# Performance work log

Hardware: AMD Instinct MI355X
Metric: run time of the kernel (lower is better)

## Reference

```python
import jax, jax.numpy as jnp
import numpy as np

N_HEAD = 16
MAX_WAVELENGTH = 10000
ROPE_PCT = 1.0


def apply_p_rope(inputs, positions, head_dim, max_wavelength=MAX_WAVELENGTH, rope_percentage=ROPE_PCT):
    # inputs: [..., T, D], positions: [T]
    rope_angles = int(rope_percentage * head_dim // 2)
    nope_angles = head_dim // 2 - rope_angles
    fraction = 2.0 * jnp.arange(0, rope_angles) / head_dim
    timescale = max_wavelength ** fraction
    timescale = jnp.pad(timescale, (0, nope_angles), mode='constant', constant_values=(0, jnp.inf))
    sinusoid_inp = positions[..., None] / timescale[None, :]  # [T, D/2]
    sin = jnp.sin(sinusoid_inp)
    cos = jnp.cos(sinusoid_inp)
    first_half, second_half = jnp.split(inputs, 2, axis=-1)
    first_part = first_half * cos - second_half * sin
    second_part = second_half * cos + first_half * sin
    return jnp.concatenate([first_part, second_part], axis=-1).astype(inputs.dtype)


def setup_inputs() -> dict:
    key = jax.random.key(0)
    ks = jax.random.split(key, 4)
    B, T, C = 2, 2048, 1024
    x = jax.random.normal(ks[0], (B, T, C), dtype=jnp.float32)
    W_attn = jax.random.normal(ks[1], (C, 3 * C), dtype=jnp.float32) * 0.02
    b_attn = jnp.zeros((3 * C,), dtype=jnp.float32)
    W_proj = jax.random.normal(ks[2], (C, C), dtype=jnp.float32) * 0.02
    b_proj = jnp.zeros((C,), dtype=jnp.float32)
    return {"x": x, "W_attn": W_attn, "b_attn": b_attn, "W_proj": W_proj, "b_proj": b_proj}


def reference(x, W_attn, b_attn, W_proj, b_proj):
    B, T, C = x.shape
    H = N_HEAD
    D = C // H  # head_dim
    qkv = x @ W_attn + b_attn                     # [B, T, 3C]
    q, k, v = jnp.split(qkv, 3, axis=-1)
    def split_heads(t):
        return t.reshape(B, T, H, D).transpose(0, 2, 1, 3)  # [B, H, T, D]
    q, k, v = split_heads(q), split_heads(k), split_heads(v)
    positions = jnp.arange(T, dtype=q.dtype)
    q = apply_p_rope(q, positions, D)
    k = apply_p_rope(k, positions, D)
    scale = jnp.sqrt(D).astype(k.dtype)
    attn = jnp.einsum('bhqd,bhkd->bhqk', q, k) / scale  # [B, H, T, T]
    causal_mask = jnp.tril(jnp.ones((T, T))).astype(bool)
    attn = jnp.where(causal_mask, attn, jnp.finfo(attn.dtype).min)
    attn = jax.nn.softmax(attn, axis=-1)
    y = jnp.einsum('bhqk,bhkd->bhqd', attn, v)    # [B, H, T, D]
    y = y.transpose(0, 2, 1, 3).reshape(B, T, C)
    return y @ W_proj + b_proj
```

## Files before the change

### kernel.cpp

```cpp
#include <hip/hip_runtime.h>
#include <hip/hip_bf16.h>

typedef short short8 __attribute__((ext_vector_type(8)));
typedef float f32x4 __attribute__((ext_vector_type(4)));
typedef __hip_bfloat16 bf16;

#define MFMA(a, b, c) __builtin_amdgcn_mfma_f32_16x16x32_bf16(a, b, c, 0, 0, 0)
#define EXP2(x) __builtin_amdgcn_exp2f(x)

__device__ __forceinline__ void async16(const void* g, void* l) {
  __builtin_amdgcn_global_load_lds((const __attribute__((address_space(1))) void*)g,
                                   (__attribute__((address_space(3))) void*)l, 16, 0, 0);
}

__device__ __forceinline__ short f2bs(float x) {
  bf16 h = __float2bfloat16(x);
  return __builtin_bit_cast(short, h);
}
__device__ __forceinline__ unsigned pk2(float lo, float hi) {
  return ((unsigned)(unsigned short)f2bs(hi) << 16) | (unsigned)(unsigned short)f2bs(lo);
}

__launch_bounds__(256)
__global__ void prep(const float* __restrict__ Wa, bf16* __restrict__ WaT,
                     const float* __restrict__ Wp, bf16* __restrict__ WpT,
                     const float* __restrict__ x, bf16* __restrict__ xb,
                     float2* __restrict__ tab) {
  __shared__ __align__(16) short Ts[64 * 72];
  int id = blockIdx.x;
  int tid = threadIdx.x;
  if (id < 1024) {
    const float* src; bf16* dst; int R, Cc, bx, by;
    if (id < 768) { src = Wa; dst = WaT; R = 1024; Cc = 3072; bx = id % 48; by = id / 48; }
    else { int r = id - 768; src = Wp; dst = WpT; R = 1024; Cc = 1024; bx = r & 15; by = r >> 4; }
    int r0 = by * 64, c0 = bx * 64;
#pragma unroll
    for (int c = 0; c < 4; ++c) {
      int g = c * 1024 + tid * 4;
      int rr = g >> 6, cc = g & 63;
      float4 v = *(const float4*)(src + (size_t)(r0 + rr) * Cc + c0 + cc);
      Ts[rr * 72 + cc + 0] = f2bs(v.x);
      Ts[rr * 72 + cc + 1] = f2bs(v.y);
      Ts[rr * 72 + cc + 2] = f2bs(v.z);
      Ts[rr * 72 + cc + 3] = f2bs(v.w);
    }
    __syncthreads();
#pragma unroll
    for (int c = 0; c < 2; ++c) {
      int g = c * 2048 + tid * 8;
      int co = g >> 6, ro = g & 63;
      short8 vv;
#pragma unroll
      for (int jj = 0; jj < 8; ++jj) vv[jj] = Ts[(ro + jj) * 72 + co];
      *(short8*)(dst + (size_t)(c0 + co) * R + r0 + ro) = vv;
    }
  } else {
    int cid = id - 1024;
    int i0 = (cid * 256 + tid) * 8;
    float4 a = *(const float4*)(x + i0);
    float4 b = *(const float4*)(x + i0 + 4);
    short8 o;
    o[0] = f2bs(a.x); o[1] = f2bs(a.y); o[2] = f2bs(a.z); o[3] = f2bs(a.w);
    o[4] = f2bs(b.x); o[5] = f2bs(b.y); o[6] = f2bs(b.z); o[7] = f2bs(b.w);
    *(short8*)((short*)xb + i0) = o;
    if (cid < 256) {
      int idx = cid * 256 + tid;
      int t = idx >> 5, d = idx & 31;
      float inv = powf(10000.0f, -(float)d * (1.0f / 32.0f));
      float ang = (float)t * inv;
      tab[idx] = make_float2(cosf(ang), sinf(ang));
    }
  }
}

__launch_bounds__(256)
__global__ void gemm_qkv(const bf16* __restrict__ A, const bf16* __restrict__ Bt,
                         const float* __restrict__ bias,
                         const float2* __restrict__ rope,
                         bf16* __restrict__ qp, bf16* __restrict__ kp,
                         bf16* __restrict__ vp) {
  const int K = 1024;
  __shared__ __align__(16) short As[128 * 32];
  __shared__ __align__(16) short Bs[128 * 32];
  int tid = threadIdx.x;
  int lane = tid & 63, wave = tid >> 6;
  int l = lane & 15, quad = lane >> 4;
  int wm = wave & 1, wn = wave >> 1;
  int mBase = blockIdx.y * 128, nBase = blockIdx.x * 128;

  f32x4 acc[4][4] = {};

  int r0 = tid >> 2;
  int kk = (tid & 3) * 8;
  const bf16* Ap = A + (size_t)(mBase + r0) * K + kk;
  const bf16* Bp = Bt + (size_t)(nBase + r0) * K + kk;
  short* Asp = As + tid * 8;
  short* Bsp = Bs + tid * 8;

  for (int kb = 0; kb < K / 32; ++kb) {
    __syncthreads();
    async16(Ap, Asp);
    async16(Ap + (size_t)64 * K, Asp + 2048);
    async16(Bp, Bsp);
    async16(Bp + (size_t)64 * K, Bsp + 2048);
    Ap += 32; Bp += 32;
    __syncthreads();
    short8 af[4], bfr[4];
#pragma unroll
    for (int i = 0; i < 4; ++i)
      af[i] = *(const short8*)(As + (wm * 64 + i * 16 + l) * 32 + quad * 8);
#pragma unroll
    for (int j = 0; j < 4; ++j)
      bfr[j] = *(const short8*)(Bs + (wn * 64 + j * 16 + l) * 32 + quad * 8);
#pragma unroll
    for (int i = 0; i < 4; ++i)
#pragma unroll
      for (int j = 0; j < 4; ++j)
        acc[i][j] = MFMA(af[i], bfr[j], acc[i][j]);
  }

  int nsec = nBase + wn * 64;
  float bv[4];
#pragma unroll
  for (int j = 0; j < 4; ++j) bv[j] = bias[nsec + j * 16 + l];

  int sel = nsec >> 10;
  int h = (nsec & 1023) >> 6;
  if (sel < 2) {
    bf16* dst = (sel == 0) ? qp : kp;
    float mul = (sel == 0) ? 0.18033688f : 1.0f;
#pragma unroll
    for (int i = 0; i < 4; ++i) {
#pragma unroll
      for (int reg = 0; reg < 4; ++reg) {
        int m = mBase + wm * 64 + i * 16 + quad * 4 + reg;
        int t = m & 2047, b = m >> 11;
        size_t base = ((size_t)((b * 16 + h) * 2048 + t)) * 64;
#pragma unroll
        for (int j = 0; j < 2; ++j) {
          int d = j * 16 + l;
          float x1 = acc[i][j][reg] + bv[j];
          float x2 = acc[i][j + 2][reg] + bv[j + 2];
          float2 cs = rope[t * 32 + d];
          dst[base + d]      = __float2bfloat16((x1 * cs.x - x2 * cs.y) * mul);
          dst[base + d + 32] = __float2bfloat16((x2 * cs.x + x1 * cs.y) * mul);
        }
      }
    }
  } else {
#pragma unroll
    for (int i = 0; i < 4; ++i) {
      int m0 = mBase + wm * 64 + i * 16 + quad * 4;
      int t0 = m0 & 2047, b = m0 >> 11;
#pragma unroll
      for (int j = 0; j < 4; ++j) {
        int d = j * 16 + l;
        uint2 uu;
        uu.x = pk2(acc[i][j][0] + bv[j], acc[i][j][1] + bv[j]);
        uu.y = pk2(acc[i][j][2] + bv[j], acc[i][j][3] + bv[j]);
        *(uint2*)(vp + ((size_t)((b * 16 + h) * 64 + d)) * 2048 + t0) = uu;
      }
    }
  }
}

__launch_bounds__(256)
__global__ void gemm_proj(const bf16* __restrict__ A, const bf16* __restrict__ Bt,
                          const float* __restrict__ bias, float* __restrict__ out) {
  const int K = 1024, Nn = 1024;
  __shared__ __align__(16) short As[64 * 32];
  __shared__ __align__(16) short Bs[128 * 32];
  int tid = threadIdx.x;
  int lane = tid & 63, wave = tid >> 6;
  int l = lane & 15, quad = lane >> 4;
  int mBase = blockIdx.y * 64, nBase = blockIdx.x * 128;

  f32x4 acc[4][2] = {};

  int r0 = tid >> 2;
  int kk = (tid & 3) * 8;
  const bf16* Ap = A + (size_t)(mBase + r0) * K + kk;
  const bf16* Bp = Bt + (size_t)(nBase + r0) * K + kk;
  short* Asp = As + tid * 8;
  short* Bsp = Bs + tid * 8;

  for (int kb = 0; kb < K / 32; ++kb) {
    __syncthreads();
    async16(Ap, Asp);
    async16(Bp, Bsp);
    async16(Bp + (size_t)64 * K, Bsp + 2048);
    Ap += 32; Bp += 32;
    __syncthreads();
    short8 af[4], bfr[2];
#pragma unroll
    for (int i = 0; i < 4; ++i)
      af[i] = *(const short8*)(As + (i * 16 + l) * 32 + quad * 8);
#pragma unroll
    for (int j = 0; j < 2; ++j)
      bfr[j] = *(const short8*)(Bs + (wave * 32 + j * 16 + l) * 32 + quad * 8);
#pragma unroll
    for (int i = 0; i < 4; ++i)
#pragma unroll
      for (int j = 0; j < 2; ++j)
        acc[i][j] = MFMA(af[i], bfr[j], acc[i][j]);
  }

  int nsec = nBase + wave * 32;
  float bv[2];
#pragma unroll
  for (int j = 0; j < 2; ++j) bv[j] = bias[nsec + j * 16 + l];
#pragma unroll
  for (int i = 0; i < 4; ++i)
#pragma unroll
    for (int reg = 0; reg < 4; ++reg) {
      int m = mBase + i * 16 + quad * 4 + reg;
#pragma unroll
      for (int j = 0; j < 2; ++j)
        out[(size_t)m * Nn + nsec + j * 16 + l] = acc[i][j][reg] + bv[j];
    }
}

__launch_bounds__(256)
__global__ void flash_attn(const bf16* __restrict__ q, const bf16* __restrict__ k,
                           const bf16* __restrict__ vt, bf16* __restrict__ y) {
  __shared__ __align__(16) short Ps[4 * 32 * 66];
  int tid = threadIdx.x;
  int lane = tid & 63, wave = tid >> 6;
  int l = lane & 15, quad = lane >> 4;
  int bh = blockIdx.x;
  int by = blockIdx.y;
  int qi = (by < 8) ? (15 - by) : (by - 8);
  int q0 = qi * 128;
  int bb = bh >> 4, hh = bh & 15;

  const bf16* qh = q + (size_t)bh * 2048 * 64;
  const bf16* kh = k + (size_t)bh * 2048 * 64;
  const bf16* vh = vt + (size_t)bh * 64 * 2048;

  int qrb = q0 + wave * 32;

  short8 qf[2][2];
#pragma unroll
  for (int m = 0; m < 2; ++m)
#pragma unroll
    for (int ks = 0; ks < 2; ++ks)
      qf[m][ks] = *(const short8*)(qh + (size_t)(qrb + m * 16 + l) * 64 + ks * 32 + quad * 8);

  const bf16* kfp = kh + (size_t)l * 64 + quad * 8;
  const bf16* vfp = vh + (size_t)l * 2048 + quad * 8;

  f32x4 acc[2][4] = {};
  float lr[2][4] = {{0.f, 0.f, 0.f, 0.f}, {0.f, 0.f, 0.f, 0.f}};
  short* Pw = Ps + wave * (32 * 66);
  int nkt = ((qrb + 31) >> 6) + 1;

  for (int kt = 0; kt < nkt; ++kt) {
    int kv0 = kt * 64;

    short8 kf[2][4];
#pragma unroll
    for (int ks = 0; ks < 2; ++ks)
#pragma unroll
      for (int jn = 0; jn < 4; ++jn)
        kf[ks][jn] = *(const short8*)(kfp + (size_t)(kv0 + jn * 16) * 64 + ks * 32);

    f32x4 sacc[2][4];
#pragma unroll
    for (int m = 0; m < 2; ++m)
#pragma unroll
      for (int jn = 0; jn < 4; ++jn) sacc[m][jn] = f32x4{-16.f, -16.f, -16.f, -16.f};
    bool live1 = (kv0 <= qrb + 31);
#pragma unroll
    for (int ks = 0; ks < 2; ++ks)
#pragma unroll
      for (int jn = 0; jn < 4; ++jn) {
        sacc[0][jn] = MFMA(qf[0][ks], kf[ks][jn], sacc[0][jn]);
        sacc[1][jn] = MFMA(qf[1][ks], kf[ks][jn], sacc[1][jn]);
      }

    short8 vf[2][4];
#pragma unroll
    for (int ks = 0; ks < 2; ++ks)
#pragma unroll
      for (int jd = 0; jd < 4; ++jd)
        vf[ks][jd] = *(const short8*)(vfp + (size_t)(jd * 16) * 2048 + kv0 + ks * 32);

#pragma unroll
    for (int m = 0; m < 2; ++m) {
      int qlo = qrb + m * 16;
      if (m == 0 && kv0 > qlo + 15) continue;
      bool nm = (kv0 + 63) > qlo;
#pragma unroll
      for (int reg = 0; reg < 4; ++reg) {
        int qg = qlo + quad * 4 + reg;
        int prow = (m * 16 + quad * 4 + reg) * 66 + l;
        float ps = 0.f;
#pragma unroll
        for (int jn = 0; jn < 4; ++jn) {
          float s = sacc[m][jn][reg];
          if (nm) s = (kv0 + jn * 16 + l <= qg) ? s : -1e30f;
          float p = EXP2(s);
          ps += p;
          Pw[prow + jn * 16] = f2bs(p);
        }
        lr[m][reg] += ps;
      }
    }

#pragma unroll
    for (int m = 0; m < 2; ++m) {
      if (m == 0 && kv0 > qrb + 15) continue;
      if (m == 1 && !live1) continue;
#pragma unroll
      for (int ks = 0; ks < 2; ++ks) {
        short8 pf = *(const short8*)(Pw + (m * 16 + l) * 66 + ks * 32 + quad * 8);
#pragma unroll
        for (int jd = 0; jd < 4; ++jd)
          acc[m][jd] = MFMA(pf, vf[ks][jd], acc[m][jd]);
      }
    }
  }

#pragma unroll
  for (int m = 0; m < 2; ++m) {
#pragma unroll
    for (int reg = 0; reg < 4; ++reg) {
      float s = lr[m][reg];
#pragma unroll
      for (int mm = 1; mm <= 8; mm <<= 1)
        s += __shfl_xor(s, mm, 64);
      float inv = 1.0f / s;
      int t = qrb + m * 16 + quad * 4 + reg;
      size_t yb = ((size_t)(bb * 2048 + t)) * 1024 + hh * 64;
#pragma unroll
      for (int jd = 0; jd < 4; ++jd)
        y[yb + jd * 16 + l] = __float2bfloat16(acc[m][jd][reg] * inv);
    }
  }
}

extern "C" void kernel_launch(void* const* d_in, const int* in_sizes, int n_in,
                              void* d_out, int out_size, void* d_ws, size_t ws_size,
                              hipStream_t stream) {
  const float* x  = (const float*)d_in[0];
  const float* Wa = (const float*)d_in[1];
  const float* ba = (const float*)d_in[2];
  const float* Wp = (const float*)d_in[3];
  const float* bp = (const float*)d_in[4];

  char* ws = (char*)d_ws;
  bf16*   WaT  = (bf16*)(ws);
  bf16*   WpT  = (bf16*)(ws + 6291456);
  float2* rope = (float2*)(ws + 8388608);
  bf16*   xb   = (bf16*)(ws + 8913152);
  bf16*   qw   = xb + 4194304;
  bf16*   kw   = qw + 4194304;
  bf16*   vtw  = kw + 4194304;
  bf16*   yw   = vtw + 4194304;

  prep<<<3072, 256, 0, stream>>>(Wa, WaT, Wp, WpT, x, xb, rope);
  gemm_qkv<<<dim3(24, 32), 256, 0, stream>>>(xb, WaT, ba, rope, qw, kw, vtw);
  flash_attn<<<dim3(32, 16), 256, 0, stream>>>(qw, kw, vtw, yw);
  gemm_proj<<<dim3(8, 64), 256, 0, stream>>>(yw, WpT, bp, (float*)d_out);
}
```

Measured before the change: 215.9 us.

## Split long causal rows across wave pairs and double-buffer K fragments

Reworks how flash attention divides work. The 32 heaviest 32-row query chunks are each split across two waves along the KV dimension, and the partial accumulators are merged through shared memory. The lighter chunks stay one per wave. The grid grows from 16 to 24 blocks along y. K fragments are also loaded one tile ahead in registers, and launch bounds request 3 blocks per CU, to balance the causal workload and hide global load latency. The cost is extra LDS traffic, two __syncthreads, and more register pressure. The merge appears to depend on a fixed max offset rather than a running max, so it is correct as is.

After: 323.4 us. 1.5x slower.

```diff
diff --git a/kernel.cpp b/kernel.cpp
--- a/kernel.cpp
+++ b/kernel.cpp
@@ -220,25 +220,38 @@
     }
 }
 
-__launch_bounds__(256)
+__launch_bounds__(256, 3)
 __global__ void flash_attn(const bf16* __restrict__ q, const bf16* __restrict__ k,
                            const bf16* __restrict__ vt, bf16* __restrict__ y) {
   __shared__ __align__(16) short Ps[4 * 32 * 66];
+  __shared__ float lsh[2][32];
   int tid = threadIdx.x;
   int lane = tid & 63, wave = tid >> 6;
   int l = lane & 15, quad = lane >> 4;
   int bh = blockIdx.x;
   int by = blockIdx.y;
-  int qi = (by < 8) ? (15 - by) : (by - 8);
-  int q0 = qi * 128;
   int bb = bh >> 4, hh = bh & 15;
+
+  int c, kt0, kt1; bool dbl;
+  if (by < 16) {
+    dbl = true;
+    c = 63 - (by * 2 + (wave >> 1));
+    int nkt = (c >> 1) + 1;
+    int h = nkt >> 1;
+    kt0 = (wave & 1) ? h : 0;
+    kt1 = (wave & 1) ? nkt : h;
+  } else {
+    dbl = false;
+    c = 31 - ((by - 16) * 4 + wave);
+    kt0 = 0;
+    kt1 = (c >> 1) + 1;
+  }
+  int qrb = c * 32;
 
   const bf16* qh = q + (size_t)bh * 2048 * 64;
   const bf16* kh = k + (size_t)bh * 2048 * 64;
   const bf16* vh = vt + (size_t)bh * 64 * 2048;
 
-  int qrb = q0 + wave * 32;
-
   short8 qf[2][2];
 #pragma unroll
   for (int m = 0; m < 2; ++m)
@@ -252,18 +265,19 @@
   f32x4 acc[2][4] = {};
   float lr[2][4] = {{0.f, 0.f, 0.f, 0.f}, {0.f, 0.f, 0.f, 0.f}};
   short* Pw = Ps + wave * (32 * 66);
-  int nkt = ((qrb + 31) >> 6) + 1;
-
-  for (int kt = 0; kt < nkt; ++kt) {
+
+  short8 kfA[2][4], kfB[2][4];
+  auto loadk = [&](short8 (&kf)[2][4], int kt) {
     int kv0 = kt * 64;
-
-    short8 kf[2][4];
 #pragma unroll
     for (int ks = 0; ks < 2; ++ks)
 #pragma unroll
       for (int jn = 0; jn < 4; ++jn)
         kf[ks][jn] = *(const short8*)(kfp + (size_t)(kv0 + jn * 16) * 64 + ks * 32);
-
+  };
+
+  auto tile = [&](const short8 (&kf)[2][4], int kt) {
+    int kv0 = kt * 64;
     f32x4 sacc[2][4];
 #pragma unroll
     for (int m = 0; m < 2; ++m)
@@ -319,22 +333,72 @@
           acc[m][jd] = MFMA(pf, vf[ks][jd], acc[m][jd]);
       }
     }
-  }
-
-#pragma unroll
-  for (int m = 0; m < 2; ++m) {
+  };
+
+  loadk(kfA, kt0);
+  for (int kt = kt0; kt < kt1; kt += 2) {
+    if (kt + 1 < kt1) loadk(kfB, kt + 1);
+    tile(kfA, kt);
+    if (kt + 1 < kt1) {
+      if (kt + 2 < kt1) loadk(kfA, kt + 2);
+      tile(kfB, kt + 1);
+    }
+  }
+
+#pragma unroll
+  for (int m = 0; m < 2; ++m)
 #pragma unroll
     for (int reg = 0; reg < 4; ++reg) {
       float s = lr[m][reg];
 #pragma unroll
       for (int mm = 1; mm <= 8; mm <<= 1)
         s += __shfl_xor(s, mm, 64);
-      float inv = 1.0f / s;
-      int t = qrb + m * 16 + quad * 4 + reg;
-      size_t yb = ((size_t)(bb * 2048 + t)) * 1024 + hh * 64;
-#pragma unroll
-      for (int jd = 0; jd < 4; ++jd)
-        y[yb + jd * 16 + l] = __float2bfloat16(acc[m][jd][reg] * inv);
+      lr[m][reg] = s;
+    }
+
+  if (!dbl) {
+#pragma unroll
+    for (int m = 0; m < 2; ++m)
+#pragma unroll
+      for (int reg = 0; reg < 4; ++reg) {
+        float inv = 1.0f / lr[m][reg];
+        int t = qrb + m * 16 + quad * 4 + reg;
+        size_t yb = ((size_t)(bb * 2048 + t)) * 1024 + hh * 64;
+#pragma unroll
+        for (int jd = 0; jd < 4; ++jd)
+          y[yb + jd * 16 + l] = __float2bfloat16(acc[m][jd][reg] * inv);
+      }
+  } else {
+    float* cb = (float*)Ps;
+    int p = wave >> 1;
+    __syncthreads();
+    if (wave & 1) {
+#pragma unroll
+      for (int m = 0; m < 2; ++m)
+#pragma unroll
+        for (int reg = 0; reg < 4; ++reg) {
+          int row = m * 16 + quad * 4 + reg;
+#pragma unroll
+          for (int jd = 0; jd < 4; ++jd)
+            cb[p * 2048 + row * 64 + jd * 16 + l] = acc[m][jd][reg];
+          if (l == 0) lsh[p][row] = lr[m][reg];
+        }
+    }
+    __syncthreads();
+    if (!(wave & 1)) {
+#pragma unroll
+      for (int m = 0; m < 2; ++m)
+#pragma unroll
+        for (int reg = 0; reg < 4; ++reg) {
+          int row = m * 16 + quad * 4 + reg;
+          float inv = 1.0f / (lr[m][reg] + lsh[p][row]);
+          int t = qrb + row;
+          size_t yb = ((size_t)(bb * 2048 + t)) * 1024 + hh * 64;
+#pragma unroll
+          for (int jd = 0; jd < 4; ++jd)
+            y[yb + jd * 16 + l] = __float2bfloat16(
+                (acc[m][jd][reg] + cb[p * 2048 + row * 64 + jd * 16 + l]) * inv);
+        }
     }
   }
 }
@@ -360,6 +424,6 @@
 
   prep<<<3072, 256, 0, stream>>>(Wa, WaT, Wp, WpT, x, xb, rope);
   gemm_qkv<<<dim3(24, 32), 256, 0, stream>>>(xb, WaT, ba, rope, qw, kw, vtw);
-  flash_attn<<<dim3(32, 16), 256, 0, stream>>>(qw, kw, vtw, yw);
+  flash_attn<<<dim3(32, 24), 256, 0, stream>>>(qw, kw, vtw, yw);
   gemm_proj<<<dim3(8, 64), 256, 0, stream>>>(yw, WpT, bp, (float*)d_out);
 }
```

## Balance causal attention work by pairing query chunks and splitting KV tiles across waves

Applied to the files above, without the earlier changes.

Each block now processes a short and a long 32-row query chunk, sized so that every block does the same total number of KV tiles under the causal mask. Within a block, pairs of waves split the KV tiles by parity (split-K). The partial accumulators and row sums are then combined through shared memory, reusing the P buffer, before the output is written. This removes the work imbalance between waves and blocks in the causal loop. In exchange it adds extra __syncthreads, LDS traffic for the combine, and half the waves sit idle while the output is written.

After: 218.9 us. Within noise of the previous version (+1.4%).

```diff
diff --git a/kernel.cpp b/kernel.cpp
--- a/kernel.cpp
+++ b/kernel.cpp
@@ -224,119 +224,169 @@
 __global__ void flash_attn(const bf16* __restrict__ q, const bf16* __restrict__ k,
                            const bf16* __restrict__ vt, bf16* __restrict__ y) {
   __shared__ __align__(16) short Ps[4 * 32 * 66];
+  __shared__ float lsh[2][32];
   int tid = threadIdx.x;
   int lane = tid & 63, wave = tid >> 6;
   int l = lane & 15, quad = lane >> 4;
   int bh = blockIdx.x;
   int by = blockIdx.y;
-  int qi = (by < 8) ? (15 - by) : (by - 8);
-  int q0 = qi * 128;
   int bb = bh >> 4, hh = bh & 15;
+  int pairId = wave >> 1, par = wave & 1;
+
+  int cS = (by << 1) | pairId;
+  int cL = 63 - cS;
 
   const bf16* qh = q + (size_t)bh * 2048 * 64;
   const bf16* kh = k + (size_t)bh * 2048 * 64;
   const bf16* vh = vt + (size_t)bh * 64 * 2048;
 
-  int qrb = q0 + wave * 32;
-
-  short8 qf[2][2];
-#pragma unroll
-  for (int m = 0; m < 2; ++m)
-#pragma unroll
-    for (int ks = 0; ks < 2; ++ks)
-      qf[m][ks] = *(const short8*)(qh + (size_t)(qrb + m * 16 + l) * 64 + ks * 32 + quad * 8);
-
   const bf16* kfp = kh + (size_t)l * 64 + quad * 8;
   const bf16* vfp = vh + (size_t)l * 2048 + quad * 8;
 
-  f32x4 acc[2][4] = {};
-  float lr[2][4] = {{0.f, 0.f, 0.f, 0.f}, {0.f, 0.f, 0.f, 0.f}};
   short* Pw = Ps + wave * (32 * 66);
-  int nkt = ((qrb + 31) >> 6) + 1;
-
-  for (int kt = 0; kt < nkt; ++kt) {
-    int kv0 = kt * 64;
-
-    short8 kf[2][4];
-#pragma unroll
-    for (int ks = 0; ks < 2; ++ks)
-#pragma unroll
-      for (int jn = 0; jn < 4; ++jn)
-        kf[ks][jn] = *(const short8*)(kfp + (size_t)(kv0 + jn * 16) * 64 + ks * 32);
-
-    f32x4 sacc[2][4];
+  float* cb = (float*)Ps + pairId * 2048;
+
+  f32x4 acc[2][4];
+  float lr[2][4];
+
+  auto run_chunk = [&](int qrb, int nkt) {
+    short8 qf[2][2];
 #pragma unroll
     for (int m = 0; m < 2; ++m)
 #pragma unroll
-      for (int jn = 0; jn < 4; ++jn) sacc[m][jn] = f32x4{-16.f, -16.f, -16.f, -16.f};
-    bool live1 = (kv0 <= qrb + 31);
-#pragma unroll
-    for (int ks = 0; ks < 2; ++ks)
-#pragma unroll
-      for (int jn = 0; jn < 4; ++jn) {
-        sacc[0][jn] = MFMA(qf[0][ks], kf[ks][jn], sacc[0][jn]);
-        sacc[1][jn] = MFMA(qf[1][ks], kf[ks][jn], sacc[1][jn]);
+      for (int ks = 0; ks < 2; ++ks)
+        qf[m][ks] = *(const short8*)(qh + (size_t)(qrb + m * 16 + l) * 64 + ks * 32 + quad * 8);
+
+    for (int kt = par; kt < nkt; kt += 2) {
+      int kv0 = kt * 64;
+
+      short8 kf[2][4];
+#pragma unroll
+      for (int ks = 0; ks < 2; ++ks)
+#pragma unroll
+        for (int jn = 0; jn < 4; ++jn)
+          kf[ks][jn] = *(const short8*)(kfp + (size_t)(kv0 + jn * 16) * 64 + ks * 32);
+
+      f32x4 sacc[2][4];
+#pragma unroll
+      for (int m = 0; m < 2; ++m)
+#pragma unroll
+        for (int jn = 0; jn < 4; ++jn) sacc[m][jn] = f32x4{-16.f, -16.f, -16.f, -16.f};
+#pragma unroll
+      for (int ks = 0; ks < 2; ++ks)
+#pragma unroll
+        for (int jn = 0; jn < 4; ++jn) {
+          sacc[0][jn] = MFMA(qf[0][ks], kf[ks][jn], sacc[0][jn]);
+          sacc[1][jn] = MFMA(qf[1][ks], kf[ks][jn], sacc[1][jn]);
+        }
+
+      short8 vf[2][4];
+#pragma unroll
+      for (int ks = 0; ks < 2; ++ks)
+#pragma unroll
+        for (int jd = 0; jd < 4; ++jd)
+          vf[ks][jd] = *(const short8*)(vfp + (size_t)(jd * 16) * 2048 + kv0 + ks * 32);
+
+#pragma unroll
+      for (int m = 0; m < 2; ++m) {
+        int qlo = qrb + m * 16;
+        if (m == 0 && kv0 > qlo + 15) continue;
+        bool nm = (kv0 + 63) > qlo;
+#pragma unroll
+        for (int reg = 0; reg < 4; ++reg) {
+          int qg = qlo + quad * 4 + reg;
+          int prow = (m * 16 + quad * 4 + reg) * 66 + l;
+          float ps = 0.f;
+#pragma unroll
+          for (int jn = 0; jn < 4; ++jn) {
+            float s = sacc[m][jn][reg];
+            if (nm) s = (kv0 + jn * 16 + l <= qg) ? s : -1e30f;
+            float p = EXP2(s);
+            ps += p;
+            Pw[prow + jn * 16] = f2bs(p);
+          }
+          lr[m][reg] += ps;
+        }
       }
 
-    short8 vf[2][4];
-#pragma unroll
-    for (int ks = 0; ks < 2; ++ks)
-#pragma unroll
-      for (int jd = 0; jd < 4; ++jd)
-        vf[ks][jd] = *(const short8*)(vfp + (size_t)(jd * 16) * 2048 + kv0 + ks * 32);
-
-#pragma unroll
-    for (int m = 0; m < 2; ++m) {
-      int qlo = qrb + m * 16;
-      if (m == 0 && kv0 > qlo + 15) continue;
-      bool nm = (kv0 + 63) > qlo;
+#pragma unroll
+      for (int m = 0; m < 2; ++m) {
+        if (m == 0 && kv0 > qrb + 15) continue;
+#pragma unroll
+        for (int ks = 0; ks < 2; ++ks) {
+          short8 pf = *(const short8*)(Pw + (m * 16 + l) * 66 + ks * 32 + quad * 8);
+#pragma unroll
+          for (int jd = 0; jd < 4; ++jd)
+            acc[m][jd] = MFMA(pf, vf[ks][jd], acc[m][jd]);
+        }
+      }
+    }
+  };
+
+  auto combine_write = [&](int qrb) {
+#pragma unroll
+    for (int m = 0; m < 2; ++m)
 #pragma unroll
       for (int reg = 0; reg < 4; ++reg) {
-        int qg = qlo + quad * 4 + reg;
-        int prow = (m * 16 + quad * 4 + reg) * 66 + l;
-        float ps = 0.f;
-#pragma unroll
-        for (int jn = 0; jn < 4; ++jn) {
-          float s = sacc[m][jn][reg];
-          if (nm) s = (kv0 + jn * 16 + l <= qg) ? s : -1e30f;
-          float p = EXP2(s);
-          ps += p;
-          Pw[prow + jn * 16] = f2bs(p);
-        }
-        lr[m][reg] += ps;
+        float s = lr[m][reg];
+#pragma unroll
+        for (int mm = 1; mm <= 8; mm <<= 1)
+          s += __shfl_xor(s, mm, 64);
+        lr[m][reg] = s;
       }
-    }
-
-#pragma unroll
-    for (int m = 0; m < 2; ++m) {
-      if (m == 0 && kv0 > qrb + 15) continue;
-      if (m == 1 && !live1) continue;
-#pragma unroll
-      for (int ks = 0; ks < 2; ++ks) {
-        short8 pf = *(const short8*)(Pw + (m * 16 + l) * 66 + ks * 32 + quad * 8);
-#pragma unroll
-        for (int jd = 0; jd < 4; ++jd)
-          acc[m][jd] = MFMA(pf, vf[ks][jd], acc[m][jd]);
-      }
-    }
-  }
-
-#pragma unroll
-  for (int m = 0; m < 2; ++m) {
-#pragma unroll
-    for (int reg = 0; reg < 4; ++reg) {
-      float s = lr[m][reg];
-#pragma unroll
-      for (int mm = 1; mm <= 8; mm <<= 1)
-        s += __shfl_xor(s, mm, 64);
-      float inv = 1.0f / s;
-      int t = qrb + m * 16 + quad * 4 + reg;
-      size_t yb = ((size_t)(bb * 2048 + t)) * 1024 + hh * 64;
-#pragma unroll
-      for (int jd = 0; jd < 4; ++jd)
-        y[yb + jd * 16 + l] = __float2bfloat16(acc[m][jd][reg] * inv);
-    }
-  }
+    __syncthreads();
+    if (par) {
+#pragma unroll
+      for (int m = 0; m < 2; ++m)
+#pragma unroll
+        for (int reg = 0; reg < 4; ++reg) {
+          int row = m * 16 + quad * 4 + reg;
+#pragma unroll
+          for (int jd = 0; jd < 4; ++jd)
+            cb[row * 64 + jd * 16 + l] = acc[m][jd][reg];
+          if (l == 0) lsh[pairId][row] = lr[m][reg];
+        }
+    }
+    __syncthreads();
+    if (!par) {
+#pragma unroll
+      for (int m = 0; m < 2; ++m)
+#pragma unroll
+        for (int reg = 0; reg < 4; ++reg) {
+          int row = m * 16 + quad * 4 + reg;
+          float inv = 1.0f / (lr[m][reg] + lsh[pairId][row]);
+          int t = qrb + row;
+          size_t yb = ((size_t)(bb * 2048 + t)) * 1024 + hh * 64;
+#pragma unroll
+          for (int jd = 0; jd < 4; ++jd)
+            y[yb + jd * 16 + l] = __float2bfloat16(
+                (acc[m][jd][reg] + cb[row * 64 + jd * 16 + l]) * inv);
+        }
+    }
+    __syncthreads();
+  };
+
+#pragma unroll
+  for (int m = 0; m < 2; ++m)
+#pragma unroll
+    for (int reg = 0; reg < 4; ++reg) { lr[m][reg] = 0.f; }
+#pragma unroll
+  for (int m = 0; m < 2; ++m)
+#pragma unroll
+    for (int jd = 0; jd < 4; ++jd) acc[m][jd] = f32x4{0.f, 0.f, 0.f, 0.f};
+  run_chunk(cS * 32, by + 1);
+  combine_write(cS * 32);
+
+#pragma unroll
+  for (int m = 0; m < 2; ++m)
+#pragma unroll
+    for (int reg = 0; reg < 4; ++reg) { lr[m][reg] = 0.f; }
+#pragma unroll
+  for (int m = 0; m < 2; ++m)
+#pragma unroll
+    for (int jd = 0; jd < 4; ++jd) acc[m][jd] = f32x4{0.f, 0.f, 0.f, 0.f};
+  run_chunk(cL * 32, 32 - by);
+  combine_write(cL * 32);
 }
 
 extern "C" void kernel_launch(void* const* d_in, const int* in_sizes, int n_in,
```

## Stage K/V tiles through double-buffered LDS with async loads in flash attention

Applied to the files above, without the earlier changes.

Instead of each wave loading its K and V fragments straight from global memory, the block now copies each 64-row K and V^T tile into LDS with async global-to-LDS loads. Two buffers let the next tile load while the current one is used, and an XOR swizzle keeps the LDS reads free of bank conflicts. The four waves share one staged tile, so each K/V byte is fetched from global memory once per block instead of once per wave. In exchange it adds about 32KB of LDS and two block-wide barriers per step, which may lower occupancy and makes waves that have finished their causal work wait for the others.

After: 219.6 us. Within noise of the previous version (+1.7%).

```diff
diff --git a/kernel.cpp b/kernel.cpp
--- a/kernel.cpp
+++ b/kernel.cpp
@@ -223,6 +223,8 @@
 __launch_bounds__(256)
 __global__ void flash_attn(const bf16* __restrict__ q, const bf16* __restrict__ k,
                            const bf16* __restrict__ vt, bf16* __restrict__ y) {
+  __shared__ __align__(16) short Kb[2][64 * 64];
+  __shared__ __align__(16) short Vb[2][64 * 64];
   __shared__ __align__(16) short Ps[4 * 32 * 66];
   int tid = threadIdx.x;
   int lane = tid & 63, wave = tid >> 6;
@@ -246,79 +248,110 @@
     for (int ks = 0; ks < 2; ++ks)
       qf[m][ks] = *(const short8*)(qh + (size_t)(qrb + m * 16 + l) * 64 + ks * 32 + quad * 8);
 
-  const bf16* kfp = kh + (size_t)l * 64 + quad * 8;
-  const bf16* vfp = vh + (size_t)l * 2048 + quad * 8;
+  int r0s = tid >> 3, p0s = tid & 7;
+  int r1s = r0s + 32;
+  const bf16* ksrc0 = kh + (size_t)r0s * 64 + (p0s ^ (r0s & 7)) * 8;
+  const bf16* ksrc1 = kh + (size_t)r1s * 64 + (p0s ^ (r1s & 7)) * 8;
+  const bf16* vsrc0 = vh + (size_t)r0s * 2048 + (p0s ^ (r0s & 7)) * 8;
+  const bf16* vsrc1 = vh + (size_t)r1s * 2048 + (p0s ^ (r1s & 7)) * 8;
+
+  auto stage = [&](int buf, int kv0) {
+    short* kd = Kb[buf] + tid * 8;
+    short* vd = Vb[buf] + tid * 8;
+    async16(ksrc0 + (size_t)kv0 * 64, kd);
+    async16(ksrc1 + (size_t)kv0 * 64, kd + 2048);
+    async16(vsrc0 + kv0, vd);
+    async16(vsrc1 + kv0, vd + 2048);
+  };
 
   f32x4 acc[2][4] = {};
   float lr[2][4] = {{0.f, 0.f, 0.f, 0.f}, {0.f, 0.f, 0.f, 0.f}};
   short* Pw = Ps + wave * (32 * 66);
-  int nkt = ((qrb + 31) >> 6) + 1;
-
-  for (int kt = 0; kt < nkt; ++kt) {
-    int kv0 = kt * 64;
-
-    short8 kf[2][4];
-#pragma unroll
-    for (int ks = 0; ks < 2; ++ks)
-#pragma unroll
-      for (int jn = 0; jn < 4; ++jn)
-        kf[ks][jn] = *(const short8*)(kfp + (size_t)(kv0 + jn * 16) * 64 + ks * 32);
-
-    f32x4 sacc[2][4];
-#pragma unroll
-    for (int m = 0; m < 2; ++m)
-#pragma unroll
-      for (int jn = 0; jn < 4; ++jn) sacc[m][jn] = f32x4{-16.f, -16.f, -16.f, -16.f};
-    bool live1 = (kv0 <= qrb + 31);
-#pragma unroll
-    for (int ks = 0; ks < 2; ++ks)
-#pragma unroll
-      for (int jn = 0; jn < 4; ++jn) {
-        sacc[0][jn] = MFMA(qf[0][ks], kf[ks][jn], sacc[0][jn]);
-        sacc[1][jn] = MFMA(qf[1][ks], kf[ks][jn], sacc[1][jn]);
+  int nsteps = 2 * qi + 2;
+
+  stage(0, 0);
+  for (int s = 0; s < nsteps; ++s) {
+    if (s + 1 < nsteps) {
+      stage((s + 1) & 1, (s + 1) * 64);
+      asm volatile("s_waitcnt vmcnt(4)" ::: "memory");
+    } else {
+      asm volatile("s_waitcnt vmcnt(0)" ::: "memory");
+    }
+    __builtin_amdgcn_s_barrier();
+
+    int kv0 = s * 64;
+    if (kv0 <= qrb + 31) {
+      const short* Kc = Kb[s & 1];
+      const short* Vc = Vb[s & 1];
+
+      short8 kf[2][4];
+#pragma unroll
+      for (int ks = 0; ks < 2; ++ks)
+#pragma unroll
+        for (int jn = 0; jn < 4; ++jn) {
+          int row = jn * 16 + l;
+          kf[ks][jn] = *(const short8*)(Kc + row * 64 + (((ks << 2) + quad) ^ (row & 7)) * 8);
+        }
+
+      f32x4 sacc[2][4];
+#pragma unroll
+      for (int m = 0; m < 2; ++m)
+#pragma unroll
+        for (int jn = 0; jn < 4; ++jn) sacc[m][jn] = f32x4{-16.f, -16.f, -16.f, -16.f};
+#pragma unroll
+      for (int ks = 0; ks < 2; ++ks)
+#pragma unroll
+        for (int jn = 0; jn < 4; ++jn) {
+          sacc[0][jn] = MFMA(qf[0][ks], kf[ks][jn], sacc[0][jn]);
+          sacc[1][jn] = MFMA(qf[1][ks], kf[ks][jn], sacc[1][jn]);
+        }
+
+      short8 vf[2][4];
+#pragma unroll
+      for (int ks = 0; ks < 2; ++ks)
+#pragma unroll
+        for (int jd = 0; jd < 4; ++jd) {
+          int row = jd * 16 + l;
+          vf[ks][jd] = *(const short8*)(Vc + row * 64 + (((ks << 2) + quad) ^ (row & 7)) * 8);
+        }
+
+#pragma unroll
+      for (int m = 0; m < 2; ++m) {
+        int qlo = qrb + m * 16;
+        if (m == 0 && kv0 > qlo + 15) continue;
+        bool nm = (kv0 + 63) > qlo;
+#pragma unroll
+        for (int reg = 0; reg < 4; ++reg) {
+          int qg = qlo + quad * 4 + reg;
+          int prow = (m * 16 + quad * 4 + reg) * 66 + l;
+          float ps = 0.f;
+#pragma unroll
+          for (int jn = 0; jn < 4; ++jn) {
+            float s2 = sacc[m][jn][reg];
+            if (nm) s2 = (kv0 + jn * 16 + l <= qg) ? s2 : -1e30f;
+            float p = EXP2(s2);
+            ps += p;
+            Pw[prow + jn * 16] = f2bs(p);
+          }
+          lr[m][reg] += ps;
+        }
       }
 
-    short8 vf[2][4];
-#pragma unroll
-    for (int ks = 0; ks < 2; ++ks)
-#pragma unroll
-      for (int jd = 0; jd < 4; ++jd)
-        vf[ks][jd] = *(const short8*)(vfp + (size_t)(jd * 16) * 2048 + kv0 + ks * 32);
-
-#pragma unroll
-    for (int m = 0; m < 2; ++m) {
-      int qlo = qrb + m * 16;
-      if (m == 0 && kv0 > qlo + 15) continue;
-      bool nm = (kv0 + 63) > qlo;
-#pragma unroll
-      for (int reg = 0; reg < 4; ++reg) {
-        int qg = qlo + quad * 4 + reg;
-        int prow = (m * 16 + quad * 4 + reg) * 66 + l;
-        float ps = 0.f;
-#pragma unroll
-        for (int jn = 0; jn < 4; ++jn) {
-          float s = sacc[m][jn][reg];
-          if (nm) s = (kv0 + jn * 16 + l <= qg) ? s : -1e30f;
-          float p = EXP2(s);
-          ps += p;
-          Pw[prow + jn * 16] = f2bs(p);
-        }
-        lr[m][reg] += ps;
+#pragma unroll
+      for (int m = 0; m < 2; ++m) {
+        if (m == 0 && kv0 > qrb + 15) continue;
+#pragma unroll
+        for (int ks = 0; ks < 2; ++ks) {
+          short8 pf = *(const short8*)(Pw + (m * 16 + l) * 66 + ks * 32 + quad * 8);
+#pragma unroll
+          for (int jd = 0; jd < 4; ++jd)
+            acc[m][jd] = MFMA(pf, vf[ks][jd], acc[m][jd]);
+        }
       }
     }
 
-#pragma unroll
-    for (int m = 0; m < 2; ++m) {
-      if (m == 0 && kv0 > qrb + 15) continue;
-      if (m == 1 && !live1) continue;
-#pragma unroll
-      for (int ks = 0; ks < 2; ++ks) {
-        short8 pf = *(const short8*)(Pw + (m * 16 + l) * 66 + ks * 32 + quad * 8);
-#pragma unroll
-        for (int jd = 0; jd < 4; ++jd)
-          acc[m][jd] = MFMA(pf, vf[ks][jd], acc[m][jd]);
-      }
-    }
+    asm volatile("" ::: "memory");
+    __builtin_amdgcn_s_barrier();
   }
 
 #pragma unroll
```
